# Performance work log

Measured on AMD Instinct MI355X. Metric: run time of the kernel, lower is better.

## Reference

```python
import jax, jax.numpy as jnp
import numpy as np

EMBED_DIM = 1024
NUM_HEADS = 16
HEAD_DIM = EMBED_DIM // NUM_HEADS


def setup_inputs() -> dict:
    key = jax.random.key(0)
    ks = jax.random.split(key, 12)
    B, S, E = 2, 2048, EMBED_DIM
    scale = 1.0 / np.sqrt(E)
    inp = {
        "query": jax.random.normal(ks[0], (B, S, E), dtype=jnp.float32),
        "key": jax.random.normal(ks[1], (B, S, E), dtype=jnp.float32),
        "value": jax.random.normal(ks[2], (B, S, E), dtype=jnp.float32),
        "key_padding_mask": jax.random.randint(ks[3], (B, S), 0, 2).astype(bool),
        # Linear params (torch nn.Linear: y = x @ W.T + b)
        "Wq": jax.random.normal(ks[4], (E, E), dtype=jnp.float32) * scale,
        "bq": jnp.zeros((E,), dtype=jnp.float32),
        "Wk": jax.random.normal(ks[5], (E, E), dtype=jnp.float32) * scale,
        "bk": jnp.zeros((E,), dtype=jnp.float32),
        "Wv": jax.random.normal(ks[6], (E, E), dtype=jnp.float32) * scale,
        "bv": jnp.zeros((E,), dtype=jnp.float32),
        "Wo": jax.random.normal(ks[7], (E, E), dtype=jnp.float32) * scale,
        "bo": jnp.zeros((E,), dtype=jnp.float32),
    }
    return inp


def reference(query, key, value, key_padding_mask, Wq, bq, Wk, bk, Wv, bv, Wo, bo):
    B, Sq, E = query.shape
    H, D = NUM_HEADS, HEAD_DIM

    def split_heads(x, W, b):
        y = x @ W.T + b                      # [B, S, E]
        return y.reshape(B, -1, H, D).transpose(0, 2, 1, 3)  # [B, H, S, D]

    q = split_heads(query, Wq, bq)
    k = split_heads(key, Wk, bk)
    v = split_heads(value, Wv, bv)

    scores = jnp.einsum("bhqd,bhkd->bhqk", q, k) / jnp.sqrt(jnp.float32(D))
    scores = jnp.where(key_padding_mask[:, None, None, :], -jnp.inf, scores)
    probs = jax.nn.softmax(scores, axis=-1)  # dropout p=0.0 -> identity
    attn = jnp.einsum("bhqk,bhkd->bhqd", probs, v)
    attn = attn.transpose(0, 2, 1, 3).reshape(B, Sq, E)
    return attn @ Wo.T + bo
```

## Files before the change

kernel.cpp:

```cpp
#include <hip/hip_runtime.h>
#include <hip/hip_bf16.h>

#define BATCH 2
#define SEQ   2048
#define EMBED 1024
#define NHEAD 16
#define HDIM  64

typedef __bf16 bf16x8 __attribute__((ext_vector_type(8)));
typedef __bf16 bf16x4 __attribute__((ext_vector_type(4)));
typedef float  floatx4 __attribute__((ext_vector_type(4)));

struct ConvAll { const void* src[7]; void* dst[7]; unsigned n[7]; };

__device__ __forceinline__ int derive_isbf(const void* qptr) {
    const unsigned short* u = (const unsigned short*)qptr;
    int sane = 0;
    for (int k = 0; k < 64; ++k) {
        int e = (u[2 * k] >> 7) & 0xff;
        if (e >= 117 && e <= 137) sane++;
    }
    return (sane >= 40) ? 1 : 0;
}

__global__ __launch_bounds__(256) void prep_convert(
        ConvAll a, const void* qptr, const void* mptr,
        int* flags, __hip_bfloat16* mones) {
    if (blockIdx.y == 7) {
        if (blockIdx.x >= 16) return;
        const unsigned int* w = (const unsigned int*)mptr;
        int all01 = 1, allf = 1;
        for (int i = 0; i < 64; ++i) {
            unsigned int x = w[i];
            if (!(x == 0u || x == 1u)) all01 = 0;
            if (!(x == 0u || x == 0x3F800000u)) allf = 0;
        }
        const int bytemask = (all01 || allf) ? 0 : 1;
        const int i = blockIdx.x * 256 + threadIdx.x;
        int v;
        if (bytemask) v = (((const unsigned char*)mptr)[i] != 0);
        else          v = (((const unsigned int*)mptr)[i] != 0u);
        mones[i] = __float2bfloat16(v ? 0.f : 1.f);
        if (blockIdx.x == 0 && threadIdx.x == 0) {
            flags[0] = derive_isbf(qptr);
            flags[1] = bytemask;
        }
        return;
    }
    if (derive_isbf(qptr)) return;
    const int t = blockIdx.y;
    const unsigned n8 = a.n[t] / 8;
    const unsigned stride = gridDim.x * blockDim.x;
    for (unsigned i = blockIdx.x * blockDim.x + threadIdx.x; i < n8; i += stride) {
        const unsigned base = i * 8;
        const float* s = (const float*)a.src[t] + base;
        __hip_bfloat16 tmp[8];
#pragma unroll
        for (int j = 0; j < 8; ++j) tmp[j] = __float2bfloat16(s[j]);
        *(uint4*)((__hip_bfloat16*)a.dst[t] + base) = *(const uint4*)tmp;
    }
}

__device__ __forceinline__ void gload_lds16(const __hip_bfloat16* g, __bf16* l) {
    __builtin_amdgcn_global_load_lds(
        (const __attribute__((address_space(1))) unsigned int*)g,
        (__attribute__((address_space(3))) unsigned int*)l, 16, 0, 0);
}

struct GemmIO {
    const void* Xr; const __hip_bfloat16* Xc;
    const void* Wr; const __hip_bfloat16* Wc;
    const void* br;
    void* Y;
    float osc;
};
struct GemmArgs { GemmIO io[3]; };

__global__ __launch_bounds__(256, 2) void gemm_mfma(
        GemmArgs args, int M, int N, int K, const int* flags,
        const __hip_bfloat16* __restrict__ mones) {
    const GemmIO io = args.io[blockIdx.z];
    const int isbf = flags[0];
    const __hip_bfloat16* Xp = isbf ? (const __hip_bfloat16*)io.Xr : io.Xc;
    const __hip_bfloat16* Wp = isbf ? (const __hip_bfloat16*)io.Wr : io.Wc;
    __shared__ __bf16 Xs[128 * 64];
    __shared__ __bf16 Ws[128 * 64];
    const int lane = threadIdx.x & 63, wv = threadIdx.x >> 6;
    const int wr = wv >> 1, wc = wv & 1;
    const int l = lane & 15, quad = lane >> 4;

    const int lin = blockIdx.x + blockIdx.y * 8;
    const int tsw = (lin & 7) * 32 + (lin >> 3);
    const int row0 = (tsw >> 3) * 128, col0 = (tsw & 7) * 128;

    const int srow = lane >> 3;
    const int schunk = (lane & 7) ^ srow;
    const __hip_bfloat16* xbase = Xp + (size_t)(row0 + srow) * K + schunk * 8;
    const __hip_bfloat16* wbase = Wp + (size_t)(col0 + srow) * K + schunk * 8;

    floatx4 acc[4][4] = {};

    for (int k0 = 0; k0 < K; k0 += 64) {
        __syncthreads();
#pragma unroll
        for (int i = 0; i < 4; ++i) {
            const int instr = wv * 4 + i;
            gload_lds16(xbase + (size_t)instr * 8 * K + k0, &Xs[instr * 512]);
        }
#pragma unroll
        for (int i = 0; i < 4; ++i) {
            const int instr = wv * 4 + i;
            gload_lds16(wbase + (size_t)instr * 8 * K + k0, &Ws[instr * 512]);
        }
        __syncthreads();
#pragma unroll
        for (int kk = 0; kk < 2; ++kk) {
            bf16x8 af[4], bfr[4];
#pragma unroll
            for (int m = 0; m < 4; ++m)
                af[m] = *(const bf16x8*)
                    &Xs[(wr * 64 + m * 16 + l) * 64 + ((kk * 4 + quad) ^ (l & 7)) * 8];
#pragma unroll
            for (int n = 0; n < 4; ++n)
                bfr[n] = *(const bf16x8*)
                    &Ws[(wc * 64 + n * 16 + l) * 64 + ((kk * 4 + quad) ^ (l & 7)) * 8];
#pragma unroll
            for (int m = 0; m < 4; ++m)
#pragma unroll
                for (int n = 0; n < 4; ++n)
                    acc[m][n] = __builtin_amdgcn_mfma_f32_16x16x32_bf16(
                        af[m], bfr[n], acc[m][n], 0, 0, 0);
        }
    }

    if (blockIdx.z == 2) {
#pragma unroll
        for (int m = 0; m < 4; ++m) {
            const int rb = row0 + wr * 64 + m * 16 + quad * 4;
            const int b = rb >> 11, s0 = rb & (SEQ - 1);
            float mf[4];
#pragma unroll
            for (int r = 0; r < 4; ++r)
                mf[r] = __bfloat162float(mones[rb + r]);
#pragma unroll
            for (int n = 0; n < 4; ++n) {
                const int col = col0 + wc * 64 + n * 16 + l;
                const int h = col >> 6, d = col & 63;
                const float bv = isbf
                    ? __bfloat162float(((const __hip_bfloat16*)io.br)[col])
                    : ((const float*)io.br)[col];
                bf16x4 out;
#pragma unroll
                for (int r = 0; r < 4; ++r)
                    out[r] = (__bf16)((acc[m][n][r] + bv) * mf[r]);
                *(bf16x4*)((__hip_bfloat16*)io.Y +
                           ((size_t)((b << 4) + h) * HDIM + d) * SEQ + s0) = out;
            }
        }
    } else {
#pragma unroll
        for (int m = 0; m < 4; ++m) {
#pragma unroll
            for (int n = 0; n < 4; ++n) {
                const int col = col0 + wc * 64 + n * 16 + l;
                const float bv = isbf
                    ? __bfloat162float(((const __hip_bfloat16*)io.br)[col])
                    : ((const float*)io.br)[col];
#pragma unroll
                for (int r = 0; r < 4; ++r) {
                    const int row = row0 + wr * 64 + m * 16 + quad * 4 + r;
                    const float v = (acc[m][n][r] + bv) * io.osc;
                    ((__hip_bfloat16*)io.Y)[(size_t)row * N + col] = __float2bfloat16(v);
                }
            }
        }
    }
}

__global__ __launch_bounds__(256, 2) void gemm_out(
        const __hip_bfloat16* __restrict__ X,
        const void* __restrict__ Wr, const __hip_bfloat16* __restrict__ Wc,
        const void* __restrict__ bias, void* __restrict__ Y,
        const int* flags) {
    const int N = EMBED, K = EMBED;
    const int isbf = flags[0];
    const __hip_bfloat16* Wp = isbf ? (const __hip_bfloat16*)Wr : Wc;
    __shared__ __bf16 Xs[64 * 64];
    __shared__ __bf16 Ws[128 * 64];
    const int lane = threadIdx.x & 63, wv = threadIdx.x >> 6;
    const int wr = wv >> 1, wc = wv & 1;
    const int l = lane & 15, quad = lane >> 4;

    const int lin = blockIdx.x + blockIdx.y * 8;
    const int tsw = (lin & 7) * 64 + (lin >> 3);
    const int row0 = (tsw >> 3) * 64, col0 = (tsw & 7) * 128;

    const int srow = lane >> 3;
    const int schunk = (lane & 7) ^ srow;
    const __hip_bfloat16* xbase = X + (size_t)(row0 + srow) * K + schunk * 8;
    const __hip_bfloat16* wbase = Wp + (size_t)(col0 + srow) * K + schunk * 8;

    floatx4 acc[2][4] = {};

    for (int k0 = 0; k0 < K; k0 += 64) {
        __syncthreads();
#pragma unroll
        for (int i = 0; i < 2; ++i) {
            const int instr = wv * 2 + i;
            gload_lds16(xbase + (size_t)instr * 8 * K + k0, &Xs[instr * 512]);
        }
#pragma unroll
        for (int i = 0; i < 4; ++i) {
            const int instr = wv * 4 + i;
            gload_lds16(wbase + (size_t)instr * 8 * K + k0, &Ws[instr * 512]);
        }
        __syncthreads();
#pragma unroll
        for (int kk = 0; kk < 2; ++kk) {
            bf16x8 af[2], bfr[4];
#pragma unroll
            for (int m = 0; m < 2; ++m)
                af[m] = *(const bf16x8*)
                    &Xs[(wr * 32 + m * 16 + l) * 64 + ((kk * 4 + quad) ^ (l & 7)) * 8];
#pragma unroll
            for (int n = 0; n < 4; ++n)
                bfr[n] = *(const bf16x8*)
                    &Ws[(wc * 64 + n * 16 + l) * 64 + ((kk * 4 + quad) ^ (l & 7)) * 8];
#pragma unroll
            for (int m = 0; m < 2; ++m)
#pragma unroll
                for (int n = 0; n < 4; ++n)
                    acc[m][n] = __builtin_amdgcn_mfma_f32_16x16x32_bf16(
                        af[m], bfr[n], acc[m][n], 0, 0, 0);
        }
    }

#pragma unroll
    for (int m = 0; m < 2; ++m) {
#pragma unroll
        for (int n = 0; n < 4; ++n) {
            const int col = col0 + wc * 64 + n * 16 + l;
            const float bv = isbf
                ? __bfloat162float(((const __hip_bfloat16*)bias)[col])
                : ((const float*)bias)[col];
#pragma unroll
            for (int r = 0; r < 4; ++r) {
                const int row = row0 + wr * 32 + m * 16 + quad * 4 + r;
                const float v = acc[m][n][r] + bv;
                if (isbf)
                    ((__hip_bfloat16*)Y)[(size_t)row * N + col] = __float2bfloat16(v);
                else
                    ((float*)Y)[(size_t)row * N + col] = v;
            }
        }
    }
}

__global__ __launch_bounds__(256) void attn_mfma(
        const __hip_bfloat16* __restrict__ Qb,
        const __hip_bfloat16* __restrict__ Kb,
        const __hip_bfloat16* __restrict__ Vt,
        const __hip_bfloat16* __restrict__ mones,
        __hip_bfloat16* __restrict__ Ao) {
    const int bh = blockIdx.x, b = bh >> 4, h = bh & 15;
    const int q0 = blockIdx.y * 128;
    const int wv = threadIdx.x >> 6, lane = threadIdx.x & 63;
    const int l = lane & 15, quad = lane >> 4;

    __shared__ __bf16 Ks[2][128 * 64];
    __shared__ __bf16 Vs[2][64 * 128];

    bf16x8 aQ[2][2];
#pragma unroll
    for (int g = 0; g < 2; ++g) {
        const int qrow = q0 + wv * 32 + g * 16 + l;
        const __hip_bfloat16* qp =
            Qb + ((size_t)(b * SEQ + qrow)) * EMBED + h * HDIM + quad * 8;
        aQ[g][0] = *(const bf16x8*)qp;
        aQ[g][1] = *(const bf16x8*)(qp + 32);
    }

    floatx4 O[2][4] = {};
    floatx4 Ol[2] = {};
    const int rho = 8 * (l >> 2) + (l & 3);

    const int ksrow = lane >> 3, kpc = lane & 7;
    const int vsrow = lane >> 4, vpc = lane & 15;
    const __hip_bfloat16* mbase = mones + b * SEQ;

    auto stage = [&](int k0, int buf) {
#pragma unroll
        for (int i = 0; i < 4; ++i) {
            const int row = wv * 32 + i * 8 + ksrow;
            const int sc = kpc ^ ((row & 3) | (((row >> 3) & 1) << 2));
            gload_lds16(Kb + ((size_t)(b * SEQ + k0 + row)) * EMBED + h * HDIM +
                            sc * 8,
                        &Ks[buf][(wv * 32 + i * 8) * 64]);
        }
#pragma unroll
        for (int i = 0; i < 4; ++i) {
            const int row = wv * 16 + i * 4 + vsrow;
            const int sc = vpc ^ (row & 15);
            gload_lds16(Vt + ((size_t)(bh * HDIM + row)) * SEQ + k0 + sc * 8,
                        &Vs[buf][(wv * 16 + i * 4) * 128]);
        }
    };

    auto compute = [&](int k0, int buf) {
#pragma unroll
        for (int kh2 = 0; kh2 < 2; ++kh2) {
            bf16x8 a0[4], a1[4];
#pragma unroll
            for (int n = 0; n < 4; ++n) {
                const int rr = kh2 * 64 + 32 * (n >> 1) + 4 * (n & 1) + rho;
                const int f = (rr & 3) | (((rr >> 3) & 1) << 2);
                a0[n] = *(const bf16x8*)&Ks[buf][rr * 64 + ((quad) ^ f) * 8];
                a1[n] = *(const bf16x8*)&Ks[buf][rr * 64 + ((quad + 4) ^ f) * 8];
            }
            bf16x8 bv[2][4];
#pragma unroll
            for (int kh = 0; kh < 2; ++kh)
#pragma unroll
                for (int dt = 0; dt < 4; ++dt) {
                    const int c = kh2 * 8 + kh * 4 + quad;
                    bv[kh][dt] = *(const bf16x8*)
                        &Vs[buf][(dt * 16 + l) * 128 + (c ^ l) * 8];
                }
            bf16x8 vm[2];
#pragma unroll
            for (int kh = 0; kh < 2; ++kh)
                vm[kh] = *(const bf16x8*)
                    (mbase + k0 + kh2 * 64 + kh * 32 + quad * 8);

#pragma unroll
            for (int g = 0; g < 2; ++g) {
                floatx4 S[4];
                __builtin_amdgcn_s_setprio(1);
#pragma unroll
                for (int n = 0; n < 4; ++n) {
                    floatx4 c = {};
                    c = __builtin_amdgcn_mfma_f32_16x16x32_bf16(a0[n], aQ[g][0],
                                                                c, 0, 0, 0);
                    c = __builtin_amdgcn_mfma_f32_16x16x32_bf16(a1[n], aQ[g][1],
                                                                c, 0, 0, 0);
                    S[n] = c;
                }
                __builtin_amdgcn_s_setprio(0);
#pragma unroll
                for (int n = 0; n < 4; ++n)
#pragma unroll
                    for (int r = 0; r < 4; ++r)
                        S[n][r] = __builtin_amdgcn_exp2f(S[n][r]);
#pragma unroll
                for (int kh = 0; kh < 2; ++kh) {
                    bf16x8 ap;
#pragma unroll
                    for (int j = 0; j < 4; ++j) {
                        ap[j]     = (__bf16)S[2 * kh][j];
                        ap[j + 4] = (__bf16)S[2 * kh + 1][j];
                    }
                    __builtin_amdgcn_s_setprio(1);
#pragma unroll
                    for (int dt = 0; dt < 4; ++dt)
                        O[g][dt] = __builtin_amdgcn_mfma_f32_16x16x32_bf16(
                            ap, bv[kh][dt], O[g][dt], 0, 0, 0);
                    Ol[g] = __builtin_amdgcn_mfma_f32_16x16x32_bf16(
                        ap, vm[kh], Ol[g], 0, 0, 0);
                    __builtin_amdgcn_s_setprio(0);
                }
            }
        }
    };

    stage(0, 0);
    const int NT = SEQ / 128;
    for (int tt = 0; tt < NT; tt += 2) {
        __syncthreads();
        stage((tt + 1) * 128, 1);
        compute(tt * 128, 0);
        __syncthreads();
        if (tt + 2 < NT) stage((tt + 2) * 128, 0);
        compute((tt + 1) * 128, 1);
    }
#pragma unroll
    for (int g = 0; g < 2; ++g)
#pragma unroll
        for (int r = 0; r < 4; ++r) {
            const float lr = Ol[g][r];
            const float inv = (lr > 0.f) ? __builtin_amdgcn_rcpf(lr) : 0.f;
            const int row = q0 + wv * 32 + g * 16 + quad * 4 + r;
#pragma unroll
            for (int dt = 0; dt < 4; ++dt)
                Ao[((size_t)(b * SEQ + row)) * EMBED + h * HDIM + dt * 16 + l] =
                    __float2bfloat16(O[g][dt][r] * inv);
        }
}

extern "C" void kernel_launch(void* const* d_in, const int* in_sizes, int n_in,
                              void* d_out, int out_size, void* d_ws, size_t ws_size,
                              hipStream_t stream) {
    const void* query = d_in[0];
    const void* key   = d_in[1];
    const void* value = d_in[2];
    const void* mask  = d_in[3];

    char* ws = (char*)d_ws;
    int* flags = (int*)ws;
    __hip_bfloat16* mones = (__hip_bfloat16*)(ws + 2048);
    const size_t TEN = (size_t)BATCH * SEQ * EMBED;
    const size_t WEL = (size_t)EMBED * EMBED;
    char* p = ws + 32768;
    __hip_bfloat16* Qc  = (__hip_bfloat16*)p;  p += TEN * 2;
    __hip_bfloat16* Kc  = (__hip_bfloat16*)p;  p += TEN * 2;
    __hip_bfloat16* Vc  = (__hip_bfloat16*)p;  p += TEN * 2;
    __hip_bfloat16* Wqc = (__hip_bfloat16*)p;  p += WEL * 2;
    __hip_bfloat16* Wkc = (__hip_bfloat16*)p;  p += WEL * 2;
    __hip_bfloat16* Wvc = (__hip_bfloat16*)p;  p += WEL * 2;
    __hip_bfloat16* Woc = (__hip_bfloat16*)p;  p += WEL * 2;
    __hip_bfloat16* Qb  = (__hip_bfloat16*)p;  p += TEN * 2;
    __hip_bfloat16* Kb  = (__hip_bfloat16*)p;  p += TEN * 2;
    __hip_bfloat16* Vt  = (__hip_bfloat16*)p;  p += TEN * 2;
    __hip_bfloat16* Ao  = Qc;

    const int M = BATCH * SEQ;
    const float QSCALE = 0.125f * 1.44269504088896f;

    ConvAll ca;
    ca.src[0] = query;    ca.dst[0] = Qc;  ca.n[0] = (unsigned)TEN;
    ca.src[1] = key;      ca.dst[1] = Kc;  ca.n[1] = (unsigned)TEN;
    ca.src[2] = value;    ca.dst[2] = Vc;  ca.n[2] = (unsigned)TEN;
    ca.src[3] = d_in[4];  ca.dst[3] = Wqc; ca.n[3] = (unsigned)WEL;
    ca.src[4] = d_in[6];  ca.dst[4] = Wkc; ca.n[4] = (unsigned)WEL;
    ca.src[5] = d_in[8];  ca.dst[5] = Wvc; ca.n[5] = (unsigned)WEL;
    ca.src[6] = d_in[10]; ca.dst[6] = Woc; ca.n[6] = (unsigned)WEL;
    prep_convert<<<dim3(256, 8), 256, 0, stream>>>(ca, query, mask, flags, mones);

    GemmArgs qkv;
    qkv.io[0] = { query, Qc, d_in[4],  Wqc, d_in[5],  (void*)Qb, QSCALE };
    qkv.io[1] = { key,   Kc, d_in[6],  Wkc, d_in[7],  (void*)Kb, 1.0f };
    qkv.io[2] = { value, Vc, d_in[8],  Wvc, d_in[9],  (void*)Vt, 1.0f };
    gemm_mfma<<<dim3(EMBED / 128, M / 128, 3), 256, 0, stream>>>(
        qkv, M, EMBED, EMBED, flags, mones);

    attn_mfma<<<dim3(BATCH * NHEAD, SEQ / 128), 256, 0, stream>>>(
        Qb, Kb, Vt, mones, Ao);

    gemm_out<<<dim3(EMBED / 128, M / 64), 256, 0, stream>>>(
        Ao, d_in[10], Woc, d_in[11], d_out, flags);
}
```

Before: 215.6 us.

## Split attention query tile across 8 waves with 16 rows each

The attention kernel now launches 512 threads per block. Each of the 8 waves owns 16 query rows instead of 32, which halves per-wave accumulators and registers. The K/V staging work is also split across the 8 waves. The goal is more waves in flight to hide LDS and exp latency. In exchange, each K/V LDS fragment load feeds only one query group per wave, so LDS read traffic per MFMA doubles.

```diff
diff --git a/kernel.cpp b/kernel.cpp
--- a/kernel.cpp
+++ b/kernel.cpp
@@ -256,7 +256,7 @@
     }
 }
 
-__global__ __launch_bounds__(256) void attn_mfma(
+__global__ __launch_bounds__(512, 4) void attn_mfma(
         const __hip_bfloat16* __restrict__ Qb,
         const __hip_bfloat16* __restrict__ Kb,
         const __hip_bfloat16* __restrict__ Vt,
@@ -270,18 +270,17 @@
     __shared__ __bf16 Ks[2][128 * 64];
     __shared__ __bf16 Vs[2][64 * 128];
 
-    bf16x8 aQ[2][2];
-#pragma unroll
-    for (int g = 0; g < 2; ++g) {
-        const int qrow = q0 + wv * 32 + g * 16 + l;
+    bf16x8 aQ[2];
+    {
+        const int qrow = q0 + wv * 16 + l;
         const __hip_bfloat16* qp =
             Qb + ((size_t)(b * SEQ + qrow)) * EMBED + h * HDIM + quad * 8;
-        aQ[g][0] = *(const bf16x8*)qp;
-        aQ[g][1] = *(const bf16x8*)(qp + 32);
-    }
-
-    floatx4 O[2][4] = {};
-    floatx4 Ol[2] = {};
+        aQ[0] = *(const bf16x8*)qp;
+        aQ[1] = *(const bf16x8*)(qp + 32);
+    }
+
+    floatx4 O[4] = {};
+    floatx4 Ol = {};
     const int rho = 8 * (l >> 2) + (l & 3);
 
     const int ksrow = lane >> 3, kpc = lane & 7;
@@ -290,19 +289,19 @@
 
     auto stage = [&](int k0, int buf) {
 #pragma unroll
-        for (int i = 0; i < 4; ++i) {
-            const int row = wv * 32 + i * 8 + ksrow;
+        for (int i = 0; i < 2; ++i) {
+            const int row = wv * 16 + i * 8 + ksrow;
             const int sc = kpc ^ ((row & 3) | (((row >> 3) & 1) << 2));
             gload_lds16(Kb + ((size_t)(b * SEQ + k0 + row)) * EMBED + h * HDIM +
                             sc * 8,
-                        &Ks[buf][(wv * 32 + i * 8) * 64]);
-        }
-#pragma unroll
-        for (int i = 0; i < 4; ++i) {
-            const int row = wv * 16 + i * 4 + vsrow;
+                        &Ks[buf][(wv * 16 + i * 8) * 64]);
+        }
+#pragma unroll
+        for (int i = 0; i < 2; ++i) {
+            const int row = wv * 8 + i * 4 + vsrow;
             const int sc = vpc ^ (row & 15);
             gload_lds16(Vt + ((size_t)(bh * HDIM + row)) * SEQ + k0 + sc * 8,
-                        &Vs[buf][(wv * 16 + i * 4) * 128]);
+                        &Vs[buf][(wv * 8 + i * 4) * 128]);
         }
     };
 
@@ -332,42 +331,39 @@
                 vm[kh] = *(const bf16x8*)
                     (mbase + k0 + kh2 * 64 + kh * 32 + quad * 8);
 
-#pragma unroll
-            for (int g = 0; g < 2; ++g) {
-                floatx4 S[4];
+            floatx4 S[4];
+            __builtin_amdgcn_s_setprio(1);
+#pragma unroll
+            for (int n = 0; n < 4; ++n) {
+                floatx4 c = {};
+                c = __builtin_amdgcn_mfma_f32_16x16x32_bf16(a0[n], aQ[0],
+                                                            c, 0, 0, 0);
+                c = __builtin_amdgcn_mfma_f32_16x16x32_bf16(a1[n], aQ[1],
+                                                            c, 0, 0, 0);
+                S[n] = c;
+            }
+            __builtin_amdgcn_s_setprio(0);
+#pragma unroll
+            for (int n = 0; n < 4; ++n)
+#pragma unroll
+                for (int r = 0; r < 4; ++r)
+                    S[n][r] = __builtin_amdgcn_exp2f(S[n][r]);
+#pragma unroll
+            for (int kh = 0; kh < 2; ++kh) {
+                bf16x8 ap;
+#pragma unroll
+                for (int j = 0; j < 4; ++j) {
+                    ap[j]     = (__bf16)S[2 * kh][j];
+                    ap[j + 4] = (__bf16)S[2 * kh + 1][j];
+                }
                 __builtin_amdgcn_s_setprio(1);
 #pragma unroll
-                for (int n = 0; n < 4; ++n) {
-                    floatx4 c = {};
-                    c = __builtin_amdgcn_mfma_f32_16x16x32_bf16(a0[n], aQ[g][0],
-                                                                c, 0, 0, 0);
-                    c = __builtin_amdgcn_mfma_f32_16x16x32_bf16(a1[n], aQ[g][1],
-                                                                c, 0, 0, 0);
-                    S[n] = c;
-                }
+                for (int dt = 0; dt < 4; ++dt)
+                    O[dt] = __builtin_amdgcn_mfma_f32_16x16x32_bf16(
+                        ap, bv[kh][dt], O[dt], 0, 0, 0);
+                Ol = __builtin_amdgcn_mfma_f32_16x16x32_bf16(
+                    ap, vm[kh], Ol, 0, 0, 0);
                 __builtin_amdgcn_s_setprio(0);
-#pragma unroll
-                for (int n = 0; n < 4; ++n)
-#pragma unroll
-                    for (int r = 0; r < 4; ++r)
-                        S[n][r] = __builtin_amdgcn_exp2f(S[n][r]);
-#pragma unroll
-                for (int kh = 0; kh < 2; ++kh) {
-                    bf16x8 ap;
-#pragma unroll
-                    for (int j = 0; j < 4; ++j) {
-                        ap[j]     = (__bf16)S[2 * kh][j];
-                        ap[j + 4] = (__bf16)S[2 * kh + 1][j];
-                    }
-                    __builtin_amdgcn_s_setprio(1);
-#pragma unroll
-                    for (int dt = 0; dt < 4; ++dt)
-                        O[g][dt] = __builtin_amdgcn_mfma_f32_16x16x32_bf16(
-                            ap, bv[kh][dt], O[g][dt], 0, 0, 0);
-                    Ol[g] = __builtin_amdgcn_mfma_f32_16x16x32_bf16(
-                        ap, vm[kh], Ol[g], 0, 0, 0);
-                    __builtin_amdgcn_s_setprio(0);
-                }
             }
         }
     };
@@ -383,17 +379,15 @@
         compute((tt + 1) * 128, 1);
     }
 #pragma unroll
-    for (int g = 0; g < 2; ++g)
-#pragma unroll
-        for (int r = 0; r < 4; ++r) {
-            const float lr = Ol[g][r];
-            const float inv = (lr > 0.f) ? __builtin_amdgcn_rcpf(lr) : 0.f;
-            const int row = q0 + wv * 32 + g * 16 + quad * 4 + r;
-#pragma unroll
-            for (int dt = 0; dt < 4; ++dt)
-                Ao[((size_t)(b * SEQ + row)) * EMBED + h * HDIM + dt * 16 + l] =
-                    __float2bfloat16(O[g][dt][r] * inv);
-        }
+    for (int r = 0; r < 4; ++r) {
+        const float lr = Ol[r];
+        const float inv = (lr > 0.f) ? __builtin_amdgcn_rcpf(lr) : 0.f;
+        const int row = q0 + wv * 16 + quad * 4 + r;
+#pragma unroll
+        for (int dt = 0; dt < 4; ++dt)
+            Ao[((size_t)(b * SEQ + row)) * EMBED + h * HDIM + dt * 16 + l] =
+                __float2bfloat16(O[dt][r] * inv);
+    }
 }
 
 extern "C" void kernel_launch(void* const* d_in, const int* in_sizes, int n_in,
@@ -442,7 +436,7 @@
     gemm_mfma<<<dim3(EMBED / 128, M / 128, 3), 256, 0, stream>>>(
         qkv, M, EMBED, EMBED, flags, mones);
 
-    attn_mfma<<<dim3(BATCH * NHEAD, SEQ / 128), 256, 0, stream>>>(
+    attn_mfma<<<dim3(BATCH * NHEAD, SEQ / 128), 512, 0, stream>>>(
         Qb, Kb, Vt, mones, Ao);
 
     gemm_out<<<dim3(EMBED / 128, M / 64), 256, 0, stream>>>(
```

Measured after the change: 215.2 us, median of 2. No clear change (-0.2%).

## Split attention key tile across two wave groups with LDS reduction

Applied to the files above, without the earlier changes.

Doubles the attention block to 512 threads. Each group of four waves handles half of every 128-key tile, so the per-wave inner loop is halved and there are more waves per block to hide latency. The two partial O and row-sum accumulators are combined through LDS after the loop, reusing the K/V buffers. This adds an extra barrier and a reduction epilogue, and changes register and occupancy pressure through the new launch bounds.

```diff
diff --git a/kernel.cpp b/kernel.cpp
--- a/kernel.cpp
+++ b/kernel.cpp
@@ -256,7 +256,7 @@
     }
 }
 
-__global__ __launch_bounds__(256) void attn_mfma(
+__global__ __launch_bounds__(512, 4) void attn_mfma(
         const __hip_bfloat16* __restrict__ Qb,
         const __hip_bfloat16* __restrict__ Kb,
         const __hip_bfloat16* __restrict__ Vt,
@@ -265,6 +265,7 @@
     const int bh = blockIdx.x, b = bh >> 4, h = bh & 15;
     const int q0 = blockIdx.y * 128;
     const int wv = threadIdx.x >> 6, lane = threadIdx.x & 63;
+    const int qg = wv & 3, kh2 = wv >> 2;
     const int l = lane & 15, quad = lane >> 4;
 
     __shared__ __bf16 Ks[2][128 * 64];
@@ -273,7 +274,7 @@
     bf16x8 aQ[2][2];
 #pragma unroll
     for (int g = 0; g < 2; ++g) {
-        const int qrow = q0 + wv * 32 + g * 16 + l;
+        const int qrow = q0 + qg * 32 + g * 16 + l;
         const __hip_bfloat16* qp =
             Qb + ((size_t)(b * SEQ + qrow)) * EMBED + h * HDIM + quad * 8;
         aQ[g][0] = *(const bf16x8*)qp;
@@ -290,84 +291,81 @@
 
     auto stage = [&](int k0, int buf) {
 #pragma unroll
-        for (int i = 0; i < 4; ++i) {
-            const int row = wv * 32 + i * 8 + ksrow;
+        for (int i = 0; i < 2; ++i) {
+            const int row = wv * 16 + i * 8 + ksrow;
             const int sc = kpc ^ ((row & 3) | (((row >> 3) & 1) << 2));
             gload_lds16(Kb + ((size_t)(b * SEQ + k0 + row)) * EMBED + h * HDIM +
                             sc * 8,
-                        &Ks[buf][(wv * 32 + i * 8) * 64]);
-        }
-#pragma unroll
-        for (int i = 0; i < 4; ++i) {
-            const int row = wv * 16 + i * 4 + vsrow;
+                        &Ks[buf][(wv * 16 + i * 8) * 64]);
+        }
+#pragma unroll
+        for (int i = 0; i < 2; ++i) {
+            const int row = wv * 8 + i * 4 + vsrow;
             const int sc = vpc ^ (row & 15);
             gload_lds16(Vt + ((size_t)(bh * HDIM + row)) * SEQ + k0 + sc * 8,
-                        &Vs[buf][(wv * 16 + i * 4) * 128]);
+                        &Vs[buf][(wv * 8 + i * 4) * 128]);
         }
     };
 
     auto compute = [&](int k0, int buf) {
-#pragma unroll
-        for (int kh2 = 0; kh2 < 2; ++kh2) {
-            bf16x8 a0[4], a1[4];
+        bf16x8 a0[4], a1[4];
+#pragma unroll
+        for (int n = 0; n < 4; ++n) {
+            const int rr = kh2 * 64 + 32 * (n >> 1) + 4 * (n & 1) + rho;
+            const int f = (rr & 3) | (((rr >> 3) & 1) << 2);
+            a0[n] = *(const bf16x8*)&Ks[buf][rr * 64 + ((quad) ^ f) * 8];
+            a1[n] = *(const bf16x8*)&Ks[buf][rr * 64 + ((quad + 4) ^ f) * 8];
+        }
+        bf16x8 bv[2][4];
+#pragma unroll
+        for (int kh = 0; kh < 2; ++kh)
+#pragma unroll
+            for (int dt = 0; dt < 4; ++dt) {
+                const int c = kh2 * 8 + kh * 4 + quad;
+                bv[kh][dt] = *(const bf16x8*)
+                    &Vs[buf][(dt * 16 + l) * 128 + (c ^ l) * 8];
+            }
+        bf16x8 vm[2];
+#pragma unroll
+        for (int kh = 0; kh < 2; ++kh)
+            vm[kh] = *(const bf16x8*)
+                (mbase + k0 + kh2 * 64 + kh * 32 + quad * 8);
+
+#pragma unroll
+        for (int g = 0; g < 2; ++g) {
+            floatx4 S[4];
+            __builtin_amdgcn_s_setprio(1);
 #pragma unroll
             for (int n = 0; n < 4; ++n) {
-                const int rr = kh2 * 64 + 32 * (n >> 1) + 4 * (n & 1) + rho;
-                const int f = (rr & 3) | (((rr >> 3) & 1) << 2);
-                a0[n] = *(const bf16x8*)&Ks[buf][rr * 64 + ((quad) ^ f) * 8];
-                a1[n] = *(const bf16x8*)&Ks[buf][rr * 64 + ((quad + 4) ^ f) * 8];
-            }
-            bf16x8 bv[2][4];
-#pragma unroll
-            for (int kh = 0; kh < 2; ++kh)
-#pragma unroll
-                for (int dt = 0; dt < 4; ++dt) {
-                    const int c = kh2 * 8 + kh * 4 + quad;
-                    bv[kh][dt] = *(const bf16x8*)
-                        &Vs[buf][(dt * 16 + l) * 128 + (c ^ l) * 8];
+                floatx4 c = {};
+                c = __builtin_amdgcn_mfma_f32_16x16x32_bf16(a0[n], aQ[g][0],
+                                                            c, 0, 0, 0);
+                c = __builtin_amdgcn_mfma_f32_16x16x32_bf16(a1[n], aQ[g][1],
+                                                            c, 0, 0, 0);
+                S[n] = c;
+            }
+            __builtin_amdgcn_s_setprio(0);
+#pragma unroll
+            for (int n = 0; n < 4; ++n)
+#pragma unroll
+                for (int r = 0; r < 4; ++r)
+                    S[n][r] = __builtin_amdgcn_exp2f(S[n][r]);
+#pragma unroll
+            for (int kh = 0; kh < 2; ++kh) {
+                bf16x8 ap;
+#pragma unroll
+                for (int j = 0; j < 4; ++j) {
+                    ap[j]     = (__bf16)S[2 * kh][j];
+                    ap[j + 4] = (__bf16)S[2 * kh + 1][j];
                 }
-            bf16x8 vm[2];
-#pragma unroll
-            for (int kh = 0; kh < 2; ++kh)
-                vm[kh] = *(const bf16x8*)
-                    (mbase + k0 + kh2 * 64 + kh * 32 + quad * 8);
-
-#pragma unroll
-            for (int g = 0; g < 2; ++g) {
-                floatx4 S[4];
                 __builtin_amdgcn_s_setprio(1);
 #pragma unroll
-                for (int n = 0; n < 4; ++n) {
-                    floatx4 c = {};
-                    c = __builtin_amdgcn_mfma_f32_16x16x32_bf16(a0[n], aQ[g][0],
-                                                                c, 0, 0, 0);
-                    c = __builtin_amdgcn_mfma_f32_16x16x32_bf16(a1[n], aQ[g][1],
-                                                                c, 0, 0, 0);
-                    S[n] = c;
-                }
+                for (int dt = 0; dt < 4; ++dt)
+                    O[g][dt] = __builtin_amdgcn_mfma_f32_16x16x32_bf16(
+                        ap, bv[kh][dt], O[g][dt], 0, 0, 0);
+                Ol[g] = __builtin_amdgcn_mfma_f32_16x16x32_bf16(
+                    ap, vm[kh], Ol[g], 0, 0, 0);
                 __builtin_amdgcn_s_setprio(0);
-#pragma unroll
-                for (int n = 0; n < 4; ++n)
-#pragma unroll
-                    for (int r = 0; r < 4; ++r)
-                        S[n][r] = __builtin_amdgcn_exp2f(S[n][r]);
-#pragma unroll
-                for (int kh = 0; kh < 2; ++kh) {
-                    bf16x8 ap;
-#pragma unroll
-                    for (int j = 0; j < 4; ++j) {
-                        ap[j]     = (__bf16)S[2 * kh][j];
-                        ap[j + 4] = (__bf16)S[2 * kh + 1][j];
-                    }
-                    __builtin_amdgcn_s_setprio(1);
-#pragma unroll
-                    for (int dt = 0; dt < 4; ++dt)
-                        O[g][dt] = __builtin_amdgcn_mfma_f32_16x16x32_bf16(
-                            ap, bv[kh][dt], O[g][dt], 0, 0, 0);
-                    Ol[g] = __builtin_amdgcn_mfma_f32_16x16x32_bf16(
-                        ap, vm[kh], Ol[g], 0, 0, 0);
-                    __builtin_amdgcn_s_setprio(0);
-                }
             }
         }
     };
@@ -382,18 +380,44 @@
         if (tt + 2 < NT) stage((tt + 2) * 128, 0);
         compute((tt + 1) * 128, 1);
     }
-#pragma unroll
-    for (int g = 0; g < 2; ++g)
-#pragma unroll
-        for (int r = 0; r < 4; ++r) {
-            const float lr = Ol[g][r];
-            const float inv = (lr > 0.f) ? __builtin_amdgcn_rcpf(lr) : 0.f;
-            const int row = q0 + wv * 32 + g * 16 + quad * 4 + r;
+
+    __syncthreads();
+    float* cO = (float*)&Ks[0][0];
+    float* cL = (float*)&Vs[0][0];
+    if (kh2 == 1) {
+#pragma unroll
+        for (int g = 0; g < 2; ++g) {
+            const int sg = qg * 2 + g;
 #pragma unroll
             for (int dt = 0; dt < 4; ++dt)
-                Ao[((size_t)(b * SEQ + row)) * EMBED + h * HDIM + dt * 16 + l] =
-                    __float2bfloat16(O[g][dt][r] * inv);
-        }
+#pragma unroll
+                for (int r = 0; r < 4; ++r)
+                    cO[(sg * 4 + dt) * 256 + (quad * 4 + r) * 16 + l] = O[g][dt][r];
+#pragma unroll
+            for (int r = 0; r < 4; ++r)
+                cL[sg * 256 + (quad * 4 + r) * 16 + l] = Ol[g][r];
+        }
+    }
+    __syncthreads();
+    if (kh2 == 0) {
+#pragma unroll
+        for (int g = 0; g < 2; ++g) {
+            const int sg = qg * 2 + g;
+#pragma unroll
+            for (int r = 0; r < 4; ++r) {
+                const float lr = Ol[g][r] + cL[sg * 256 + (quad * 4 + r) * 16 + l];
+                const float inv = (lr > 0.f) ? __builtin_amdgcn_rcpf(lr) : 0.f;
+                const int row = q0 + qg * 32 + g * 16 + quad * 4 + r;
+#pragma unroll
+                for (int dt = 0; dt < 4; ++dt) {
+                    const float ov = O[g][dt][r] +
+                        cO[(sg * 4 + dt) * 256 + (quad * 4 + r) * 16 + l];
+                    Ao[((size_t)(b * SEQ + row)) * EMBED + h * HDIM + dt * 16 + l] =
+                        __float2bfloat16(ov * inv);
+                }
+            }
+        }
+    }
 }
 
 extern "C" void kernel_launch(void* const* d_in, const int* in_sizes, int n_in,
@@ -442,7 +466,7 @@
     gemm_mfma<<<dim3(EMBED / 128, M / 128, 3), 256, 0, stream>>>(
         qkv, M, EMBED, EMBED, flags, mones);
 
-    attn_mfma<<<dim3(BATCH * NHEAD, SEQ / 128), 256, 0, stream>>>(
+    attn_mfma<<<dim3(BATCH * NHEAD, SEQ / 128), 512, 0, stream>>>(
         Qb, Kb, Vt, mones, Ao);
 
     gemm_out<<<dim3(EMBED / 128, M / 64), 256, 0, stream>>>(
```

New measurement: 399.1 us. 85.1% more time.
